# Kernel optimization log

Hardware: AMD Instinct MI355X
Metric: run time of the kernel (lower is better)

Reference implementation:

```python
import jax, jax.numpy as jnp
import numpy as np

N_NODES = 100000
N_EDGES = 300000
HIDDEN = 256

def _lin_init(key, fan_in, fan_out):
    return jax.random.normal(key, (fan_in, fan_out), jnp.float32) / np.sqrt(fan_in)

def setup_inputs():
    key = jax.random.key(0)
    ks = jax.random.split(key, 16)
    x = jax.random.randint(ks[0], (N_NODES, 16), 0, 11).astype(jnp.float32)
    edge_index = jax.random.randint(ks[1], (2, N_EDGES), 0, N_NODES)
    edge_attr = jax.random.randint(ks[2], (N_EDGES, 4), 0, 5).astype(jnp.float32)
    batch = jnp.sort(jax.random.randint(ks[3], (N_NODES,), 0, 256))
    atom_emb = jax.random.normal(ks[4], (11, 64), jnp.float32)
    bond_emb_table = jax.random.normal(ks[5], (5, 64), jnp.float32)
    vp_w1 = _lin_init(ks[6], 64, 32); vp_b1 = jnp.zeros((32,), jnp.float32)
    vp_w2 = _lin_init(ks[7], 32, 8)
    # chemical-knowledge bias init: max_valence - 1 for atom types 0..7 (bias dim is 8)
    vp_b2 = jnp.array([3., 2., 1., 5., 0., 0., 0., 0.], jnp.float32)
    gnn_wself = jax.random.normal(ks[8], (3, HIDDEN, HIDDEN), jnp.float32) / np.sqrt(HIDDEN)
    gnn_bself = jnp.zeros((3, HIDDEN), jnp.float32)
    gnn_wmsg = jax.random.normal(ks[9], (3, HIDDEN + 64, HIDDEN), jnp.float32) / np.sqrt(HIDDEN + 64)
    gnn_bmsg = jnp.zeros((3, HIDDEN), jnp.float32)
    bc_w1 = _lin_init(ks[10], 2 * HIDDEN + 2, 128); bc_b1 = jnp.zeros((128,), jnp.float32)
    bc_w2 = _lin_init(ks[11], 128, 64); bc_b2 = jnp.zeros((64,), jnp.float32)
    bc_w3 = _lin_init(ks[12], 64, 4); bc_b3 = jnp.zeros((4,), jnp.float32)
    cp_w1 = _lin_init(ks[13], HIDDEN, 128); cp_b1 = jnp.zeros((128,), jnp.float32)
    cp_w2 = _lin_init(ks[14], 128, 32); cp_b2 = jnp.zeros((32,), jnp.float32)
    return dict(x=x, edge_attr=edge_attr, atom_emb=atom_emb, bond_emb_table=bond_emb_table,
                vp_w1=vp_w1, vp_b1=vp_b1, vp_w2=vp_w2, vp_b2=vp_b2,
                gnn_wself=gnn_wself, gnn_bself=gnn_bself, gnn_wmsg=gnn_wmsg, gnn_bmsg=gnn_bmsg,
                bc_w1=bc_w1, bc_b1=bc_b1, bc_w2=bc_w2, bc_b2=bc_b2, bc_w3=bc_w3, bc_b3=bc_b3,
                cp_w1=cp_w1, cp_b1=cp_b1, cp_w2=cp_w2, cp_b2=cp_b2,
                edge_index=edge_index, batch=batch)

def _forward(x, edge_attr, atom_emb, bond_emb_table, vp_w1, vp_b1, vp_w2, vp_b2,
             gnn_wself, gnn_bself, gnn_wmsg, gnn_bmsg,
             bc_w1, bc_b1, bc_w2, bc_b2, bc_w3, bc_b3,
             cp_w1, cp_b1, cp_w2, cp_b2, edge_index, batch):
    relu = jax.nn.relu
    n = x.shape[0]
    atom_types = jnp.clip(x[:, 0].astype(jnp.int32), 0, 10)        # [N]
    ae = atom_emb[atom_types]                                      # [N, 64]
    valence_logits = relu(ae @ vp_w1 + vp_b1) @ vp_w2 + vp_b2      # [N, 8]
    pv = jnp.argmax(valence_logits, axis=-1) + 1                   # [N] predicted valences in [1,8]
    bt = jnp.clip(edge_attr[:, 0].astype(jnp.int32), 0, 4)
    be = bond_emb_table[bt]                                        # [E, 64]
    h = jnp.concatenate([ae, jax.nn.one_hot(pv - 1, 8, dtype=ae.dtype)], axis=-1)  # [N, 72]
    h = jnp.pad(h, ((0, 0), (0, HIDDEN - h.shape[1])))             # pad to [N, HIDDEN]
    row, col = edge_index[0], edge_index[1]
    # stacked ChemicalConstraintGNN layers (message passing with bond-type features)
    for l in range(3):
        msg = relu(jnp.concatenate([h[col], be], axis=-1) @ gnn_wmsg[l] + gnn_bmsg[l])  # [E, H]
        agg = jax.ops.segment_sum(msg, row, num_segments=n)
        h = relu(h @ gnn_wself[l] + gnn_bself[l] + agg)
    # ValenceConstraintLayer: damp nodes whose degree exceeds predicted valence
    degree = jax.ops.segment_sum(jnp.ones(row.shape[0], h.dtype), row, num_segments=n)
    violations = relu(degree - pv.astype(h.dtype))                 # [N]
    h = h / (1.0 + violations)[:, None]
    # constrained bond prediction
    bf = jnp.concatenate([h[row], h[col],
                          pv[row][:, None].astype(h.dtype), pv[col][:, None].astype(h.dtype)], axis=-1)
    bl = relu(relu(bf @ bc_w1 + bc_b1) @ bc_w2 + bc_b2) @ bc_w3 + bc_b3  # [E, 4]
    # vectorized chemical constraints (replaces per-edge Python loop)
    at_r, at_c = atom_types[row], atom_types[col]
    halogen = ((at_r == 4) | (at_r == 5) | (at_c == 4) | (at_c == 5)).astype(bl.dtype)
    lowval2 = ((pv[row] <= 2) | (pv[col] <= 2)).astype(bl.dtype)
    lowval1 = ((pv[row] <= 1) | (pv[col] <= 1)).astype(bl.dtype)
    penalty = jnp.zeros_like(bl)
    penalty = penalty.at[:, 1:].add((-100.0 * halogen - 50.0 * lowval1)[:, None])
    penalty = penalty.at[:, 2].add(-50.0 * lowval2)
    bond_logits = bl + penalty
    chem_props = relu(h @ cp_w1 + cp_b1) @ cp_w2 + cp_b2           # [N, 32]
    return h, chem_props, valence_logits, bond_logits, violations

def reference(x, edge_attr, atom_emb, bond_emb_table, vp_w1, vp_b1, vp_w2, vp_b2,
              gnn_wself, gnn_bself, gnn_wmsg, gnn_bmsg,
              bc_w1, bc_b1, bc_w2, bc_b2, bc_w3, bc_b3,
              cp_w1, cp_b1, cp_w2, cp_b2, edge_index, batch):
    return _forward(x, edge_attr, atom_emb, bond_emb_table, vp_w1, vp_b1, vp_w2, vp_b2,
                    gnn_wself, gnn_bself, gnn_wmsg, gnn_bmsg,
                    bc_w1, bc_b1, bc_w2, bc_b2, bc_w3, bc_b3,
                    cp_w1, cp_b1, cp_w2, cp_b2, edge_index, batch)
```

## Files before the change

kernel.cpp:

```cpp
#include <hip/hip_runtime.h>

#define N_NODES 100000
#define N_EDGES 300000
#define M_PAD   100096
#define E_PAD   300032

typedef unsigned short u16;
typedef short bf16x8 __attribute__((ext_vector_type(8)));
typedef float f32x4  __attribute__((ext_vector_type(4)));

__device__ __forceinline__ float bf2f(u16 u) {
    unsigned x = ((unsigned)u) << 16;
    return __builtin_bit_cast(float, x);
}
__device__ __forceinline__ u16 f2bf(float f) {
    unsigned u = __builtin_bit_cast(unsigned, f);
    unsigned r = (u + 0x7FFF + ((u >> 16) & 1)) >> 16;
    return (u16)r;
}

#define H_OFF   0
#define CP_OFF  25600000
#define VL_OFF  28800000
#define BL_OFF  29600000
#define VI_OFF  30800000

#define GLL(gp, lp) __builtin_amdgcn_global_load_lds( \
    (const __attribute__((address_space(1))) unsigned int*)(gp), \
    (__attribute__((address_space(3))) unsigned int*)(lp), 16, 0, 0)

__global__ void k_type_mlp(const float* __restrict__ atom_emb,
                           const float* __restrict__ vp_w1, const float* __restrict__ vp_b1,
                           const float* __restrict__ vp_w2, const float* __restrict__ vp_b2,
                           int* __restrict__ pv_tab, float* __restrict__ vl_tab,
                           float* __restrict__ h0_tab)
{
    int tid = threadIdx.x;
    for (int i = tid; i < 11 * 256; i += 256) h0_tab[i] = 0.f;
    __syncthreads();
    if (tid < 11) {
        int t = tid;
        const float* ae = atom_emb + t * 64;
        float lg[8];
        #pragma unroll
        for (int c = 0; c < 8; ++c) lg[c] = vp_b2[c];
        for (int j = 0; j < 32; ++j) {
            float z = vp_b1[j];
            for (int d = 0; d < 64; ++d) z += ae[d] * vp_w1[d * 32 + j];
            z = fmaxf(z, 0.f);
            #pragma unroll
            for (int c = 0; c < 8; ++c) lg[c] += z * vp_w2[j * 8 + c];
        }
        int best = 0;
        #pragma unroll
        for (int c = 1; c < 8; ++c) if (lg[c] > lg[best]) best = c;
        pv_tab[t] = best + 1;
        for (int c = 0; c < 8; ++c) vl_tab[t * 8 + c] = lg[c];
        float* h0 = h0_tab + t * 256;
        for (int d = 0; d < 64; ++d) h0[d] = ae[d];
        h0[64 + best] = 1.f;
    }
}

__global__ void k_tables(const float* __restrict__ bond_emb,
                         const float* __restrict__ gnn_wself, const float* __restrict__ gnn_bself,
                         const float* __restrict__ gnn_wmsg, const float* __restrict__ gnn_bmsg,
                         const float* __restrict__ h0_tab,
                         float* __restrict__ self0_tab, float* __restrict__ msg0_tab,
                         float* __restrict__ bondtab)
{
    int b = blockIdx.x, c = threadIdx.x;
    if (b < 11) {
        int t = b;
        const float* h0 = h0_tab + t * 256;
        float acc = gnn_bself[c];
        for (int k = 0; k < 256; ++k) acc += h0[k] * gnn_wself[k * 256 + c];
        self0_tab[t * 256 + c] = acc;
    } else if (b < 66) {
        int idx = b - 11; int t = idx / 5, bb = idx % 5;
        const float* h0 = h0_tab + t * 256;
        float acc = gnn_bmsg[c];
        for (int k = 0; k < 256; ++k) acc += h0[k] * gnn_wmsg[k * 256 + c];
        const float* be = bond_emb + bb * 64;
        for (int k = 0; k < 64; ++k) acc += be[k] * gnn_wmsg[(256 + k) * 256 + c];
        msg0_tab[idx * 256 + c] = fmaxf(acc, 0.f);
    } else {
        int idx = b - 66; int l = idx / 5 + 1, bb = idx % 5;
        const float* w = gnn_wmsg + (size_t)l * 320 * 256;
        const float* be = bond_emb + bb * 64;
        float acc = gnn_bmsg[l * 256 + c];
        for (int k = 0; k < 64; ++k) acc += be[k] * w[(256 + k) * 256 + c];
        bondtab[(l - 1) * 5 * 256 + bb * 256 + c] = acc;
    }
}

__global__ void k_wtrans(const float* __restrict__ wmsg, const float* __restrict__ wself,
                         const float* __restrict__ bcw1, const float* __restrict__ cpw1,
                         const float* __restrict__ bcw2, const float* __restrict__ cpw2,
                         u16* __restrict__ BtL1, u16* __restrict__ BtL2, u16* __restrict__ Bt3,
                         u16* __restrict__ BtW2, u16* __restrict__ BtCP2)
{
    int b = blockIdx.x, k = threadIdx.x;
    if (b < 512) {
        int n = b;
        float v = (n < 256) ? wmsg[(size_t)1 * 320 * 256 + (size_t)k * 256 + n]
                            : wself[(size_t)1 * 256 * 256 + (size_t)k * 256 + (n - 256)];
        BtL1[n * 256 + k] = f2bf(v);
    } else if (b < 1024) {
        int n = b - 512;
        float v = (n < 256) ? wmsg[(size_t)2 * 320 * 256 + (size_t)k * 256 + n]
                            : wself[(size_t)2 * 256 * 256 + (size_t)k * 256 + (n - 256)];
        BtL2[n * 256 + k] = f2bf(v);
    } else if (b < 1408) {
        int n = b - 1024;
        float v;
        if (n < 128)      v = bcw1[k * 128 + n];
        else if (n < 256) v = bcw1[(256 + k) * 128 + (n - 128)];
        else              v = cpw1[k * 128 + (n - 256)];
        Bt3[n * 256 + k] = f2bf(v);
    } else if (b < 1536) {
        int n = b - 1408;
        if (k < 128) BtW2[n * 128 + k] = f2bf(n < 64 ? bcw2[k * 64 + n] : 0.f);
    } else {
        int n = b - 1536;
        if (k < 128) BtCP2[n * 128 + k] = f2bf(n < 32 ? cpw2[k * 32 + n] : 0.f);
    }
}

__global__ void k_setup_bias(const float* __restrict__ bself, const float* __restrict__ bcb1,
                             const float* __restrict__ cpb1,
                             float* __restrict__ bias512, float* __restrict__ biasPost)
{
    int i = blockIdx.x * 256 + threadIdx.x;
    if (i < 1024) {
        int l = i >> 9, c = i & 511;
        bias512[l * 512 + c] = (c < 256) ? 0.f : bself[(l + 1) * 256 + (c - 256)];
    } else if (i < 1408) {
        int c = i - 1024;
        biasPost[c] = (c < 128) ? bcb1[c] : ((c < 256) ? 0.f : cpb1[c - 256]);
    }
}

__global__ void k_node_init(const float* __restrict__ x, const int* __restrict__ pv_tab,
                            const float* __restrict__ vl_tab,
                            int* __restrict__ types, int* __restrict__ pvarr,
                            int* __restrict__ degree, float* __restrict__ vl_out)
{
    int i = blockIdx.x * blockDim.x + threadIdx.x;
    if (i >= N_NODES) return;
    int t = (int)x[i * 16];
    t = min(max(t, 0), 10);
    types[i] = t;
    pvarr[i] = pv_tab[t];
    degree[i] = 0;
    float4 v0 = *(const float4*)&vl_tab[t * 8];
    float4 v1 = *(const float4*)&vl_tab[t * 8 + 4];
    *(float4*)&vl_out[i * 8]     = v0;
    *(float4*)&vl_out[i * 8 + 4] = v1;
}

__global__ void k_edge_deg(const int* __restrict__ ei, int* __restrict__ degree)
{
    int e = blockIdx.x * blockDim.x + threadIdx.x;
    if (e >= N_EDGES) return;
    atomicAdd(&degree[ei[e]], 1);
}

#define SCAN_B 1024
__global__ void k_scan1(const int* __restrict__ degree, int* __restrict__ part, int* __restrict__ bsum)
{
    __shared__ int s[SCAN_B];
    int tid = threadIdx.x;
    int i = blockIdx.x * SCAN_B + tid;
    int v = (i < N_NODES) ? degree[i] : 0;
    s[tid] = v; __syncthreads();
    for (int off = 1; off < SCAN_B; off <<= 1) {
        int t = (tid >= off) ? s[tid - off] : 0;
        __syncthreads();
        s[tid] += t;
        __syncthreads();
    }
    if (i < N_NODES) part[i] = s[tid] - v;
    if (tid == SCAN_B - 1) bsum[blockIdx.x] = s[tid];
}

__global__ void k_scan2(const int* __restrict__ bsum, int* __restrict__ bbase, int nb)
{
    __shared__ int s[128];
    int tid = threadIdx.x;
    int v = (tid < nb) ? bsum[tid] : 0;
    s[tid] = v; __syncthreads();
    for (int off = 1; off < 128; off <<= 1) {
        int t = (tid >= off) ? s[tid - off] : 0;
        __syncthreads();
        s[tid] += t;
        __syncthreads();
    }
    bbase[tid] = s[tid] - v;
}

__global__ void k_scan3(int* __restrict__ part, const int* __restrict__ bbase, int* __restrict__ cursor)
{
    int i = blockIdx.x * SCAN_B + threadIdx.x;
    if (i >= N_NODES) return;
    int o = part[i] + bbase[blockIdx.x];
    part[i] = o;
    cursor[i] = o;
}

__global__ void k_csr_fill(const int* __restrict__ ei, const float* __restrict__ edge_attr,
                           const int* __restrict__ types, int* __restrict__ cursor,
                           int* __restrict__ csr, int* __restrict__ rowcsr, int* __restrict__ eidarr)
{
    int e = blockIdx.x * blockDim.x + threadIdx.x;
    if (e >= N_EDGES) return;
    int row = ei[e], col = ei[N_EDGES + e];
    int bt = (int)edge_attr[e * 4];
    bt = min(max(bt, 0), 4);
    int pos = atomicAdd(&cursor[row], 1);
    csr[pos] = col | (bt << 20) | (types[col] << 24);
    rowcsr[pos] = row;
    eidarr[pos] = e;
}

__global__ __launch_bounds__(256) void k_agg0(const int* __restrict__ offsets, const int* __restrict__ degree,
                       const int* __restrict__ types,
                       const float* __restrict__ self0_tab, const float* __restrict__ msg0_tab,
                       const int* __restrict__ csr, u16* __restrict__ h)
{
    int wid = threadIdx.x >> 6, lane = threadIdx.x & 63;
    int node = blockIdx.x * 4 + wid;
    if (node >= N_NODES) return;
    int t = types[node];
    float4 acc = *(const float4*)&self0_tab[t * 256 + lane * 4];
    int start = offsets[node], deg = degree[node];
    for (int j = 0; j < deg; ++j) {
        int p = csr[start + j];
        int combo = ((p >> 24) & 0xF) * 5 + ((p >> 20) & 7);
        float4 m = *(const float4*)&msg0_tab[combo * 256 + lane * 4];
        acc.x += m.x; acc.y += m.y; acc.z += m.z; acc.w += m.w;
    }
    ushort4 r;
    r.x = f2bf(fmaxf(acc.x, 0.f)); r.y = f2bf(fmaxf(acc.y, 0.f));
    r.z = f2bf(fmaxf(acc.z, 0.f)); r.w = f2bf(fmaxf(acc.w, 0.f));
    *(ushort4*)&h[(size_t)node * 256 + lane * 4] = r;
}

__global__ __launch_bounds__(256) void k_agg12(const int* __restrict__ offsets, const int* __restrict__ degree,
                        const u16* __restrict__ hs, const u16* __restrict__ hm,
                        const float* __restrict__ bondtab, const int* __restrict__ csr,
                        u16* __restrict__ h, int final_layer, const int* __restrict__ pvarr,
                        float* __restrict__ h_out, u16* __restrict__ hd_bf, float* __restrict__ viol_out)
{
    int wid = threadIdx.x >> 6, lane = threadIdx.x & 63;
    int node = blockIdx.x * 4 + wid;
    if (node >= N_NODES) return;
    ushort4 s4 = *(const ushort4*)&hs[(size_t)node * 256 + lane * 4];
    float ax = bf2f(s4.x), ay = bf2f(s4.y), az = bf2f(s4.z), aw = bf2f(s4.w);
    int start = offsets[node], deg = degree[node];
    for (int j = 0; j < deg; ++j) {
        int p = csr[start + j];
        int c = p & 0xFFFFF;
        int bt = (p >> 20) & 7;
        ushort4 m4 = *(const ushort4*)&hm[(size_t)c * 256 + lane * 4];
        float4 bb = *(const float4*)&bondtab[bt * 256 + lane * 4];
        ax += fmaxf(bf2f(m4.x) + bb.x, 0.f);
        ay += fmaxf(bf2f(m4.y) + bb.y, 0.f);
        az += fmaxf(bf2f(m4.z) + bb.z, 0.f);
        aw += fmaxf(bf2f(m4.w) + bb.w, 0.f);
    }
    ax = fmaxf(ax, 0.f); ay = fmaxf(ay, 0.f); az = fmaxf(az, 0.f); aw = fmaxf(aw, 0.f);
    if (!final_layer) {
        ushort4 r;
        r.x = f2bf(ax); r.y = f2bf(ay); r.z = f2bf(az); r.w = f2bf(aw);
        *(ushort4*)&h[(size_t)node * 256 + lane * 4] = r;
    } else {
        float viol = fmaxf((float)deg - (float)pvarr[node], 0.f);
        float s = 1.f / (1.f + viol);
        ax *= s; ay *= s; az *= s; aw *= s;
        float4 v = make_float4(ax, ay, az, aw);
        *(float4*)&h_out[(size_t)node * 256 + lane * 4] = v;
        ushort4 r;
        r.x = f2bf(ax); r.y = f2bf(ay); r.z = f2bf(az); r.w = f2bf(aw);
        *(ushort4*)&hd_bf[(size_t)node * 256 + lane * 4] = r;
        if (lane == 0) viol_out[node] = viol;
    }
}

__global__ __launch_bounds__(256) void k_gemm_dual(
    const u16* __restrict__ A, const u16* __restrict__ Bt,
    const float* __restrict__ bias512,
    u16* __restrict__ Dm, u16* __restrict__ Ds, int M, int MT)
{
    __shared__ u16 As[128 * 32];
    __shared__ u16 Bs[128 * 32];
    int b = blockIdx.x;
    int rsub = b & 31;
    int nt = rsub >> 3, m8 = rsub & 7;
    int mt = (b >> 5) * 8 + m8;
    if (mt >= MT) return;
    int bm = mt * 128, bn = nt * 128;

    int t = threadIdx.x;
    int lane = t & 63, w = t >> 6;
    int wm = w & 1, wn = w >> 1;
    f32x4 zero = {0.f, 0.f, 0.f, 0.f};
    f32x4 acc[4][4];
    #pragma unroll
    for (int i = 0; i < 4; ++i)
        #pragma unroll
        for (int j = 0; j < 4; ++j) acc[i][j] = zero;

    int arow = t >> 2, acol = (t & 3) * 8;
    const u16* Ag = A + (size_t)(bm + arow) * 256 + acol;
    const u16* Bg = Bt + (size_t)(bn + arow) * 256 + acol;
    u16* Asp = As + t * 8;
    u16* Bsp = Bs + t * 8;
    int q = lane >> 4, r = lane & 15;

    for (int k0 = 0; k0 < 256; k0 += 32) {
        __syncthreads();
        GLL(Ag + k0,            Asp);
        GLL(Ag + 64 * 256 + k0, Asp + 2048);
        GLL(Bg + k0,            Bsp);
        GLL(Bg + 64 * 256 + k0, Bsp + 2048);
        __syncthreads();
        bf16x8 af[4], bfr[4];
        #pragma unroll
        for (int i = 0; i < 4; ++i)
            af[i] = *(const bf16x8*)&As[(wm * 64 + i * 16 + r) * 32 + q * 8];
        #pragma unroll
        for (int j = 0; j < 4; ++j)
            bfr[j] = *(const bf16x8*)&Bs[(wn * 64 + j * 16 + r) * 32 + q * 8];
        #pragma unroll
        for (int i = 0; i < 4; ++i)
            #pragma unroll
            for (int j = 0; j < 4; ++j)
                acc[i][j] = __builtin_amdgcn_mfma_f32_16x16x32_bf16(af[i], bfr[j], acc[i][j], 0, 0, 0);
    }
    #pragma unroll
    for (int i = 0; i < 4; ++i) {
        int rowb = bm + wm * 64 + i * 16 + q * 4;
        #pragma unroll
        for (int j = 0; j < 4; ++j) {
            int colg = bn + wn * 64 + j * 16 + r;
            float bv = bias512[colg];
            u16* D = (colg < 256) ? Dm : Ds;
            int col = colg & 255;
            #pragma unroll
            for (int rr = 0; rr < 4; ++rr) {
                int rowg = rowb + rr;
                if (rowg < M) D[(size_t)rowg * 256 + col] = f2bf(acc[i][j][rr] + bv);
            }
        }
    }
}

__global__ __launch_bounds__(256) void k_gemm_post(
    const u16* __restrict__ A, const u16* __restrict__ Bt3,
    const float* __restrict__ biasPost,
    u16* __restrict__ UV, u16* __restrict__ CP1, int M, int MT)
{
    __shared__ u16 As[128 * 32];
    __shared__ u16 Bs[128 * 32];
    int b = blockIdx.x;
    int rsub = b % 24;
    int nt = rsub >> 3, m8 = rsub & 7;
    int mt = (b / 24) * 8 + m8;
    if (mt >= MT) return;
    int bm = mt * 128, bn = nt * 128;

    int t = threadIdx.x;
    int lane = t & 63, w = t >> 6;
    int wm = w & 1, wn = w >> 1;
    f32x4 zero = {0.f, 0.f, 0.f, 0.f};
    f32x4 acc[4][4];
    #pragma unroll
    for (int i = 0; i < 4; ++i)
        #pragma unroll
        for (int j = 0; j < 4; ++j) acc[i][j] = zero;

    int arow = t >> 2, acol = (t & 3) * 8;
    const u16* Ag = A + (size_t)(bm + arow) * 256 + acol;
    const u16* Bg = Bt3 + (size_t)(bn + arow) * 256 + acol;
    u16* Asp = As + t * 8;
    u16* Bsp = Bs + t * 8;
    int q = lane >> 4, r = lane & 15;

    for (int k0 = 0; k0 < 256; k0 += 32) {
        __syncthreads();
        GLL(Ag + k0,            Asp);
        GLL(Ag + 64 * 256 + k0, Asp + 2048);
        GLL(Bg + k0,            Bsp);
        GLL(Bg + 64 * 256 + k0, Bsp + 2048);
        __syncthreads();
        bf16x8 af[4], bfr[4];
        #pragma unroll
        for (int i = 0; i < 4; ++i)
            af[i] = *(const bf16x8*)&As[(wm * 64 + i * 16 + r) * 32 + q * 8];
        #pragma unroll
        for (int j = 0; j < 4; ++j)
            bfr[j] = *(const bf16x8*)&Bs[(wn * 64 + j * 16 + r) * 32 + q * 8];
        #pragma unroll
        for (int i = 0; i < 4; ++i)
            #pragma unroll
            for (int j = 0; j < 4; ++j)
                acc[i][j] = __builtin_amdgcn_mfma_f32_16x16x32_bf16(af[i], bfr[j], acc[i][j], 0, 0, 0);
    }
    #pragma unroll
    for (int i = 0; i < 4; ++i) {
        int rowb = bm + wm * 64 + i * 16 + q * 4;
        #pragma unroll
        for (int j = 0; j < 4; ++j) {
            int coll = wn * 64 + j * 16 + r;
            float bv = biasPost[bn + coll];
            #pragma unroll
            for (int rr = 0; rr < 4; ++rr) {
                int rowg = rowb + rr;
                if (rowg < M) {
                    float val = acc[i][j][rr] + bv;
                    if (nt < 2) UV[(size_t)rowg * 256 + bn + coll] = f2bf(val);
                    else        CP1[(size_t)rowg * 128 + coll] = f2bf(fmaxf(val, 0.f));
                }
            }
        }
    }
}

__global__ __launch_bounds__(256) void k_gemm_k128(
    const u16* __restrict__ A, const u16* __restrict__ Bt,
    const float* __restrict__ bias, float* __restrict__ C,
    int ldc, int M, int N)
{
    __shared__ u16 As[4096];
    __shared__ u16 Bs[4096];
    int t = threadIdx.x;
    int lane = t & 63, w = t >> 6;
    int wm = w & 1, wn = w >> 1;
    int bm = blockIdx.x * 128;
    int arow = t >> 2, acol = (t & 3) * 8;
    int q = lane >> 4, r = lane & 15;
    const u16* Ag = A + (size_t)(bm + arow) * 128 + acol;
    const u16* Bg = Bt + (size_t)arow * 128 + acol;
    f32x4 zero = {0.f, 0.f, 0.f, 0.f};
    f32x4 acc[4][4];
    #pragma unroll
    for (int i = 0; i < 4; ++i)
        #pragma unroll
        for (int j = 0; j < 4; ++j) acc[i][j] = zero;

    for (int kc = 0; kc < 4; ++kc) {
        __syncthreads();
        GLL(Ag + kc * 32,            As + t * 8);
        GLL(Ag + 64 * 128 + kc * 32, As + 2048 + t * 8);
        GLL(Bg + kc * 32,            Bs + t * 8);
        GLL(Bg + 64 * 128 + kc * 32, Bs + 2048 + t * 8);
        __syncthreads();
        bf16x8 af[4], bfr[4];
        #pragma unroll
        for (int i = 0; i < 4; ++i)
            af[i] = *(const bf16x8*)&As[(wm * 64 + i * 16 + r) * 32 + q * 8];
        #pragma unroll
        for (int j = 0; j < 4; ++j)
            bfr[j] = *(const bf16x8*)&Bs[(wn * 64 + j * 16 + r) * 32 + q * 8];
        #pragma unroll
        for (int i = 0; i < 4; ++i)
            #pragma unroll
            for (int j = 0; j < 4; ++j)
                acc[i][j] = __builtin_amdgcn_mfma_f32_16x16x32_bf16(af[i], bfr[j], acc[i][j], 0, 0, 0);
    }
    #pragma unroll
    for (int i = 0; i < 4; ++i) {
        int rowb = bm + wm * 64 + i * 16 + q * 4;
        #pragma unroll
        for (int j = 0; j < 4; ++j) {
            int colg = wn * 64 + j * 16 + r;
            if (colg >= N) continue;
            float bv = bias[colg];
            #pragma unroll
            for (int rr = 0; rr < 4; ++rr) {
                int rowg = rowb + rr;
                if (rowg < M) C[(size_t)rowg * ldc + colg] = acc[i][j][rr] + bv;
            }
        }
    }
}

__global__ __launch_bounds__(256) void k_bond_fused(
    const int* __restrict__ csr, const int* __restrict__ rowcsr, const int* __restrict__ eidarr,
    const int* __restrict__ types, const int* __restrict__ pvarr, const int* __restrict__ pv_tab,
    const u16* __restrict__ uv, const float* __restrict__ bc_w1,
    const u16* __restrict__ BtW2, const float* __restrict__ bc_b2,
    const float* __restrict__ bc_w3, const float* __restrict__ bc_b3,
    float* __restrict__ bl_out)
{
    __shared__ u16 T1s[16384];
    __shared__ u16 Bs[16384];
    __shared__ float w5s[128], w6s[128], W3s[256], b2s[64], b3s[4];
    __shared__ int pvts[16];

    int t = threadIdx.x;
    int p0 = blockIdx.x * 128;

    if (t < 128) { w5s[t] = bc_w1[512 * 128 + t]; w6s[t] = bc_w1[513 * 128 + t]; }
    if (t < 256) W3s[t] = bc_w3[t];
    if (t < 64) b2s[t] = bc_b2[t];
    if (t < 4)  b3s[t] = bc_b3[t];
    if (t < 11) pvts[t] = pv_tab[t];
    #pragma unroll
    for (int c = 0; c < 4; ++c) {
        GLL(BtW2 + (size_t)(t >> 2) * 128 + c * 32 + (t & 3) * 8,        Bs + c * 4096 + t * 8);
        GLL(BtW2 + (size_t)(64 + (t >> 2)) * 128 + c * 32 + (t & 3) * 8, Bs + c * 4096 + 2048 + t * 8);
    }

    int l = t >> 1;
    int half = t & 1;
    int pos = p0 + l;
    int prow = 0, pk = 0;
    if (pos < N_EDGES) { prow = rowcsr[pos]; pk = csr[pos]; }
    int pcol = pk & 0xFFFFF;
    float pvr = (float)pvarr[prow];
    __syncthreads();
    float pvc = (float)pvts[(pk >> 24) & 0xF];

    const u16* up = uv + (size_t)prow * 256 + half * 64;
    const u16* vp = uv + (size_t)pcol * 256 + 128 + half * 64;
    #pragma unroll
    for (int j = 0; j < 8; ++j) {
        int c = half * 64 + j * 8;
        ushort4 ua = *(const ushort4*)(up + j * 8);
        ushort4 ub = *(const ushort4*)(up + j * 8 + 4);
        ushort4 va = *(const ushort4*)(vp + j * 8);
        ushort4 vb = *(const ushort4*)(vp + j * 8 + 4);
        int chunk = c >> 5, kk = c & 31;
        u16* dst = T1s + chunk * 4096 + l * 32 + kk;
        dst[0] = f2bf(fmaxf(bf2f(ua.x) + bf2f(va.x) + pvr * w5s[c+0] + pvc * w6s[c+0], 0.f));
        dst[1] = f2bf(fmaxf(bf2f(ua.y) + bf2f(va.y) + pvr * w5s[c+1] + pvc * w6s[c+1], 0.f));
        dst[2] = f2bf(fmaxf(bf2f(ua.z) + bf2f(va.z) + pvr * w5s[c+2] + pvc * w6s[c+2], 0.f));
        dst[3] = f2bf(fmaxf(bf2f(ua.w) + bf2f(va.w) + pvr * w5s[c+3] + pvc * w6s[c+3], 0.f));
        dst[4] = f2bf(fmaxf(bf2f(ub.x) + bf2f(vb.x) + pvr * w5s[c+4] + pvc * w6s[c+4], 0.f));
        dst[5] = f2bf(fmaxf(bf2f(ub.y) + bf2f(vb.y) + pvr * w5s[c+5] + pvc * w6s[c+5], 0.f));
        dst[6] = f2bf(fmaxf(bf2f(ub.z) + bf2f(vb.z) + pvr * w5s[c+6] + pvc * w6s[c+6], 0.f));
        dst[7] = f2bf(fmaxf(bf2f(ub.w) + bf2f(vb.w) + pvr * w5s[c+7] + pvc * w6s[c+7], 0.f));
    }
    __syncthreads();

    int lane = t & 63, w = t >> 6;
    int wm = w & 1, wn = w >> 1;
    int q = lane >> 4, r = lane & 15;
    f32x4 zero = {0.f, 0.f, 0.f, 0.f};
    f32x4 acc[4][4];
    #pragma unroll
    for (int i = 0; i < 4; ++i)
        #pragma unroll
        for (int j = 0; j < 4; ++j) acc[i][j] = zero;
    #pragma unroll
    for (int c = 0; c < 4; ++c) {
        bf16x8 af[4], bfr[4];
        #pragma unroll
        for (int i = 0; i < 4; ++i)
            af[i] = *(const bf16x8*)&T1s[c * 4096 + (wm * 64 + i * 16 + r) * 32 + q * 8];
        #pragma unroll
        for (int j = 0; j < 4; ++j)
            bfr[j] = *(const bf16x8*)&Bs[c * 4096 + (wn * 64 + j * 16 + r) * 32 + q * 8];
        #pragma unroll
        for (int i = 0; i < 4; ++i)
            #pragma unroll
            for (int j = 0; j < 4; ++j)
                acc[i][j] = __builtin_amdgcn_mfma_f32_16x16x32_bf16(af[i], bfr[j], acc[i][j], 0, 0, 0);
    }
    __syncthreads();

    float* T2f = (float*)T1s;
    if (wn == 0) {
        #pragma unroll
        for (int i = 0; i < 4; ++i) {
            int row = wm * 64 + i * 16 + q * 4;
            #pragma unroll
            for (int j = 0; j < 4; ++j) {
                int col = j * 16 + r;
                float bv = b2s[col];
                #pragma unroll
                for (int rr = 0; rr < 4; ++rr)
                    T2f[(row + rr) * 64 + col] = fmaxf(acc[i][j][rr] + bv, 0.f);
            }
        }
    }
    __syncthreads();

    if (t < 128) {
        int pos3 = p0 + t;
        if (pos3 < N_EDGES) {
            float a0 = b3s[0], a1 = b3s[1], a2 = b3s[2], a3 = b3s[3];
            const float* trow = &T2f[t * 64];
            #pragma unroll 8
            for (int kk = 0; kk < 64; ++kk) {
                int k = (kk + t) & 63;
                float tv = trow[k];
                a0 += tv * W3s[k * 4 + 0];
                a1 += tv * W3s[k * 4 + 1];
                a2 += tv * W3s[k * 4 + 2];
                a3 += tv * W3s[k * 4 + 3];
            }
            int prow3 = rowcsr[pos3];
            int pk3 = csr[pos3];
            int tc = (pk3 >> 24) & 0xF;
            int tr = types[prow3];
            int pr = pvarr[prow3];
            int pc = pvts[tc];
            float halogen = (tr == 4 || tr == 5 || tc == 4 || tc == 5) ? 1.f : 0.f;
            float l1 = (pr <= 1 || pc <= 1) ? 1.f : 0.f;
            float l2 = (pr <= 2 || pc <= 2) ? 1.f : 0.f;
            float pen13 = -100.f * halogen - 50.f * l1;
            a1 += pen13;
            a3 += pen13;
            a2 += pen13 - 50.f * l2;
            int eid = eidarr[pos3];
            *(float4*)&bl_out[(size_t)eid * 4] = make_float4(a0, a1, a2, a3);
        }
    }
}

extern "C" void kernel_launch(void* const* d_in, const int* in_sizes, int n_in,
                              void* d_out, int out_size, void* d_ws, size_t ws_size,
                              hipStream_t stream)
{
    const float* x          = (const float*)d_in[0];
    const float* edge_attr  = (const float*)d_in[1];
    const float* atom_emb   = (const float*)d_in[2];
    const float* bond_emb   = (const float*)d_in[3];
    const float* vp_w1      = (const float*)d_in[4];
    const float* vp_b1      = (const float*)d_in[5];
    const float* vp_w2      = (const float*)d_in[6];
    const float* vp_b2      = (const float*)d_in[7];
    const float* gnn_wself  = (const float*)d_in[8];
    const float* gnn_bself  = (const float*)d_in[9];
    const float* gnn_wmsg   = (const float*)d_in[10];
    const float* gnn_bmsg   = (const float*)d_in[11];
    const float* bc_w1      = (const float*)d_in[12];
    const float* bc_b1      = (const float*)d_in[13];
    const float* bc_w2      = (const float*)d_in[14];
    const float* bc_b2      = (const float*)d_in[15];
    const float* bc_w3      = (const float*)d_in[16];
    const float* bc_b3      = (const float*)d_in[17];
    const float* cp_w1      = (const float*)d_in[18];
    const float* cp_b1      = (const float*)d_in[19];
    const float* cp_w2      = (const float*)d_in[20];
    const float* cp_b2      = (const float*)d_in[21];
    const int*   ei         = (const int*)d_in[22];

    float* out    = (float*)d_out;
    float* h_out  = out + H_OFF;
    float* cp_out = out + CP_OFF;
    float* vl_out = out + VL_OFF;
    float* bl_out = out + BL_OFF;
    float* vi_out = out + VI_OFF;

    char* base = (char*)d_ws;
    const size_t S = (size_t)M_PAD * 256 * 2;
    u16* h_bf  = (u16*)(base + 0 * S);
    u16* uv_bf = (u16*)(base + 0 * S);
    u16* hm_bf = (u16*)(base + 1 * S);
    u16* hs_bf = (u16*)(base + 2 * S);
    u16* hd_bf = (u16*)(base + 3 * S);
    u16* cp1_bf= (u16*)(base + 4 * S);
    char* w    = base + 4 * S + (size_t)M_PAD * 128 * 2;
    int* degree  = (int*)w; w += (size_t)N_NODES * 4;
    int* offsets = (int*)w; w += (size_t)N_NODES * 4;
    int* cursor  = (int*)w; w += (size_t)N_NODES * 4;
    int* types   = (int*)w; w += (size_t)N_NODES * 4;
    int* pvarr   = (int*)w; w += (size_t)N_NODES * 4;
    int* csr     = (int*)w; w += (size_t)E_PAD * 4;
    int* rowcsr  = (int*)w; w += (size_t)E_PAD * 4;
    int* eidarr  = (int*)w; w += (size_t)E_PAD * 4;
    int* bsum    = (int*)w; w += 4096;
    int* bbase   = (int*)w; w += 4096;
    int* pv_tab  = (int*)w; w += 1024;
    float* vl_tab    = (float*)w; w += 2048;
    float* h0_tab    = (float*)w; w += 11 * 256 * 4;
    float* self0_tab = (float*)w; w += 11 * 256 * 4;
    float* msg0_tab  = (float*)w; w += 55 * 256 * 4;
    float* bondtab   = (float*)w; w += 2 * 5 * 256 * 4;
    u16* BtL1  = (u16*)w; w += 512 * 256 * 2;
    u16* BtL2  = (u16*)w; w += 512 * 256 * 2;
    u16* Bt3   = (u16*)w; w += 384 * 256 * 2;
    u16* BtW2  = (u16*)w; w += 128 * 128 * 2;
    u16* BtCP2 = (u16*)w; w += 128 * 128 * 2;
    float* bias512  = (float*)w; w += 2 * 512 * 4;
    float* biasPost = (float*)w; w += 384 * 4;

    k_type_mlp<<<1, 256, 0, stream>>>(atom_emb, vp_w1, vp_b1, vp_w2, vp_b2, pv_tab, vl_tab, h0_tab);
    k_tables<<<76, 256, 0, stream>>>(bond_emb, gnn_wself, gnn_bself, gnn_wmsg, gnn_bmsg,
                                     h0_tab, self0_tab, msg0_tab, bondtab);
    k_wtrans<<<1664, 256, 0, stream>>>(gnn_wmsg, gnn_wself, bc_w1, cp_w1, bc_w2, cp_w2,
                                       BtL1, BtL2, Bt3, BtW2, BtCP2);
    k_setup_bias<<<6, 256, 0, stream>>>(gnn_bself, bc_b1, cp_b1, bias512, biasPost);
    k_node_init<<<(N_NODES + 255) / 256, 256, 0, stream>>>(x, pv_tab, vl_tab, types, pvarr, degree, vl_out);
    k_edge_deg<<<(N_EDGES + 255) / 256, 256, 0, stream>>>(ei, degree);
    int nb = (N_NODES + SCAN_B - 1) / SCAN_B;
    k_scan1<<<nb, SCAN_B, 0, stream>>>(degree, offsets, bsum);
    k_scan2<<<1, 128, 0, stream>>>(bsum, bbase, nb);
    k_scan3<<<nb, SCAN_B, 0, stream>>>(offsets, bbase, cursor);
    k_csr_fill<<<(N_EDGES + 255) / 256, 256, 0, stream>>>(ei, edge_attr, types, cursor, csr, rowcsr, eidarr);
    k_agg0<<<N_NODES / 4, 256, 0, stream>>>(offsets, degree, types, self0_tab, msg0_tab, csr, h_bf);

    const int MT = M_PAD / 128;
    const int QB = (MT + 7) / 8;
    for (int l = 1; l <= 2; ++l) {
        const u16* BtL = (l == 1) ? BtL1 : BtL2;
        k_gemm_dual<<<QB * 32, 256, 0, stream>>>(h_bf, BtL, bias512 + (size_t)(l - 1) * 512,
                                                 hm_bf, hs_bf, N_NODES, MT);
        k_agg12<<<N_NODES / 4, 256, 0, stream>>>(offsets, degree, hs_bf, hm_bf,
                                                 bondtab + (size_t)(l - 1) * 5 * 256, csr, h_bf,
                                                 (l == 2) ? 1 : 0, pvarr, h_out, hd_bf, vi_out);
    }

    k_gemm_post<<<QB * 24, 256, 0, stream>>>(hd_bf, Bt3, biasPost, uv_bf, cp1_bf, N_NODES, MT);
    k_gemm_k128<<<MT, 256, 0, stream>>>(cp1_bf, BtCP2, cp_b2, cp_out, 32, N_NODES, 32);

    k_bond_fused<<<E_PAD / 128, 256, 0, stream>>>(csr, rowcsr, eidarr, types, pvarr, pv_tab,
                                                  uv_bf, bc_w1, BtW2, bc_b2, bc_w3, bc_b3, bl_out);
}
```

Measured before the change: 664.9 us.

## Widen GEMM K-tile to 128 with XOR-swizzled LDS layout

Both dense GEMM kernels now stage a 128-wide K slice of A and B into LDS per iteration instead of 32, which cuts the number of barrier pairs from eight to two per tile. The global-to-LDS loads use an XOR swizzle of the 16-byte chunk index by row, and the MFMA fragment reads apply the same swizzle to avoid LDS bank conflicts. LDS use per block grows from 16 KB to 64 KB, which may lower occupancy and reduce latency hiding between blocks.

```diff
diff --git a/kernel.cpp b/kernel.cpp
--- a/kernel.cpp
+++ b/kernel.cpp
@@ -292,8 +292,8 @@
     const float* __restrict__ bias512,
     u16* __restrict__ Dm, u16* __restrict__ Ds, int M, int MT)
 {
-    __shared__ u16 As[128 * 32];
-    __shared__ u16 Bs[128 * 32];
+    __shared__ u16 As[128 * 128];
+    __shared__ u16 Bs[128 * 128];
     int b = blockIdx.x;
     int rsub = b & 31;
     int nt = rsub >> 3, m8 = rsub & 7;
@@ -311,32 +311,37 @@
         #pragma unroll
         for (int j = 0; j < 4; ++j) acc[i][j] = zero;
 
-    int arow = t >> 2, acol = (t & 3) * 8;
-    const u16* Ag = A + (size_t)(bm + arow) * 256 + acol;
-    const u16* Bg = Bt + (size_t)(bn + arow) * 256 + acol;
+    int srow = t >> 4;
+    int schunk = (t & 15) ^ (srow & 15);
+    const u16* Ag = A + (size_t)(bm + srow) * 256 + schunk * 8;
+    const u16* Bg = Bt + (size_t)(bn + srow) * 256 + schunk * 8;
     u16* Asp = As + t * 8;
     u16* Bsp = Bs + t * 8;
     int q = lane >> 4, r = lane & 15;
 
-    for (int k0 = 0; k0 < 256; k0 += 32) {
-        __syncthreads();
-        GLL(Ag + k0,            Asp);
-        GLL(Ag + 64 * 256 + k0, Asp + 2048);
-        GLL(Bg + k0,            Bsp);
-        GLL(Bg + 64 * 256 + k0, Bsp + 2048);
-        __syncthreads();
-        bf16x8 af[4], bfr[4];
-        #pragma unroll
-        for (int i = 0; i < 4; ++i)
-            af[i] = *(const bf16x8*)&As[(wm * 64 + i * 16 + r) * 32 + q * 8];
-        #pragma unroll
-        for (int j = 0; j < 4; ++j)
-            bfr[j] = *(const bf16x8*)&Bs[(wn * 64 + j * 16 + r) * 32 + q * 8];
-        #pragma unroll
-        for (int i = 0; i < 4; ++i)
+    for (int k0 = 0; k0 < 256; k0 += 128) {
+        __syncthreads();
+        #pragma unroll
+        for (int g = 0; g < 8; ++g) {
+            GLL(Ag + k0 + g * 16 * 256, Asp + g * 2048);
+            GLL(Bg + k0 + g * 16 * 256, Bsp + g * 2048);
+        }
+        __syncthreads();
+        #pragma unroll
+        for (int kk = 0; kk < 4; ++kk) {
+            bf16x8 af[4], bfr[4];
+            #pragma unroll
+            for (int i = 0; i < 4; ++i)
+                af[i] = *(const bf16x8*)&As[(wm * 64 + i * 16 + r) * 128 + (((kk * 4 + q) ^ r) * 8)];
             #pragma unroll
             for (int j = 0; j < 4; ++j)
-                acc[i][j] = __builtin_amdgcn_mfma_f32_16x16x32_bf16(af[i], bfr[j], acc[i][j], 0, 0, 0);
+                bfr[j] = *(const bf16x8*)&Bs[(wn * 64 + j * 16 + r) * 128 + (((kk * 4 + q) ^ r) * 8)];
+            #pragma unroll
+            for (int i = 0; i < 4; ++i)
+                #pragma unroll
+                for (int j = 0; j < 4; ++j)
+                    acc[i][j] = __builtin_amdgcn_mfma_f32_16x16x32_bf16(af[i], bfr[j], acc[i][j], 0, 0, 0);
+        }
     }
     #pragma unroll
     for (int i = 0; i < 4; ++i) {
@@ -361,8 +366,8 @@
     const float* __restrict__ biasPost,
     u16* __restrict__ UV, u16* __restrict__ CP1, int M, int MT)
 {
-    __shared__ u16 As[128 * 32];
-    __shared__ u16 Bs[128 * 32];
+    __shared__ u16 As[128 * 128];
+    __shared__ u16 Bs[128 * 128];
     int b = blockIdx.x;
     int rsub = b % 24;
     int nt = rsub >> 3, m8 = rsub & 7;
@@ -380,32 +385,37 @@
         #pragma unroll
         for (int j = 0; j < 4; ++j) acc[i][j] = zero;
 
-    int arow = t >> 2, acol = (t & 3) * 8;
-    const u16* Ag = A + (size_t)(bm + arow) * 256 + acol;
-    const u16* Bg = Bt3 + (size_t)(bn + arow) * 256 + acol;
+    int srow = t >> 4;
+    int schunk = (t & 15) ^ (srow & 15);
+    const u16* Ag = A + (size_t)(bm + srow) * 256 + schunk * 8;
+    const u16* Bg = Bt3 + (size_t)(bn + srow) * 256 + schunk * 8;
     u16* Asp = As + t * 8;
     u16* Bsp = Bs + t * 8;
     int q = lane >> 4, r = lane & 15;
 
-    for (int k0 = 0; k0 < 256; k0 += 32) {
-        __syncthreads();
-        GLL(Ag + k0,            Asp);
-        GLL(Ag + 64 * 256 + k0, Asp + 2048);
-        GLL(Bg + k0,            Bsp);
-        GLL(Bg + 64 * 256 + k0, Bsp + 2048);
-        __syncthreads();
-        bf16x8 af[4], bfr[4];
-        #pragma unroll
-        for (int i = 0; i < 4; ++i)
-            af[i] = *(const bf16x8*)&As[(wm * 64 + i * 16 + r) * 32 + q * 8];
-        #pragma unroll
-        for (int j = 0; j < 4; ++j)
-            bfr[j] = *(const bf16x8*)&Bs[(wn * 64 + j * 16 + r) * 32 + q * 8];
-        #pragma unroll
-        for (int i = 0; i < 4; ++i)
+    for (int k0 = 0; k0 < 256; k0 += 128) {
+        __syncthreads();
+        #pragma unroll
+        for (int g = 0; g < 8; ++g) {
+            GLL(Ag + k0 + g * 16 * 256, Asp + g * 2048);
+            GLL(Bg + k0 + g * 16 * 256, Bsp + g * 2048);
+        }
+        __syncthreads();
+        #pragma unroll
+        for (int kk = 0; kk < 4; ++kk) {
+            bf16x8 af[4], bfr[4];
+            #pragma unroll
+            for (int i = 0; i < 4; ++i)
+                af[i] = *(const bf16x8*)&As[(wm * 64 + i * 16 + r) * 128 + (((kk * 4 + q) ^ r) * 8)];
             #pragma unroll
             for (int j = 0; j < 4; ++j)
-                acc[i][j] = __builtin_amdgcn_mfma_f32_16x16x32_bf16(af[i], bfr[j], acc[i][j], 0, 0, 0);
+                bfr[j] = *(const bf16x8*)&Bs[(wn * 64 + j * 16 + r) * 128 + (((kk * 4 + q) ^ r) * 8)];
+            #pragma unroll
+            for (int i = 0; i < 4; ++i)
+                #pragma unroll
+                for (int j = 0; j < 4; ++j)
+                    acc[i][j] = __builtin_amdgcn_mfma_f32_16x16x32_bf16(af[i], bfr[j], acc[i][j], 0, 0, 0);
+        }
     }
     #pragma unroll
     for (int i = 0; i < 4; ++i) {
```

Result: slower. 686.0 us (+3.2%).
